# Kernel optimization log

Measured on AMD Instinct MI355X. Metric: run time of the kernel, lower is better.

## Reference

```python
import jax, jax.numpy as jnp
import numpy as np

# levels for the auction iterations: j = 7..-1 gives level = -4^j, j = -2 gives level = 0
_LEVEL_JS = list(range(7, -3, -1))


def approx_match(xyz1, xyz2):
    # xyz1: [B,N,3], xyz2: [B,M,3] -> soft match matrix [B,N,M]
    B, N, _ = xyz1.shape
    M = xyz2.shape[1]
    multiL = 1.0 if N >= M else float(M // N)
    multiR = float(N // M) if N >= M else 1.0
    # pairwise squared distances [B,N,M]
    d2 = jnp.sum((xyz1[:, :, None, :] - xyz2[:, None, :, :]) ** 2, axis=-1)
    levels = jnp.array([0.0 if j == -2 else -(4.0 ** j) for j in _LEVEL_JS],
                       dtype=xyz1.dtype)

    def step(carry, level):
        match, remainL, remainR = carry
        w = jnp.exp(level * d2) * remainR[:, None, :]                      # [B,N,M]
        # row-normalize to each left point's remaining mass
        w = w * (remainL / (jnp.sum(w, axis=2) + 1e-9))[:, :, None]
        # clip columns to right points' remaining capacity
        ss = jnp.sum(w, axis=1) + 1e-9                                     # [B,M]
        w = w * jnp.minimum(remainR / ss, 1.0)[:, None, :]
        match = match + w
        remainL = jnp.maximum(remainL - jnp.sum(w, axis=2), 0.0)
        remainR = jnp.maximum(remainR - jnp.sum(w, axis=1), 0.0)
        return (match, remainL, remainR), None

    init = (jnp.zeros_like(d2),
            jnp.full((B, N), multiL, dtype=d2.dtype),
            jnp.full((B, M), multiR, dtype=d2.dtype))
    (match, _, _), _ = jax.lax.scan(step, init, levels)
    return match


def match_cost(xyz1, xyz2, match):
    # cost[b] = sum_{k,l} match[b,k,l] * ||xyz1[b,k] - xyz2[b,l]||
    d = jnp.sqrt(jnp.sum((xyz1[:, :, None, :] - xyz2[:, None, :, :]) ** 2, axis=-1))
    return jnp.sum(match * d, axis=(1, 2))


def setup_inputs() -> dict:
    key = jax.random.key(0)
    k1, k2 = jax.random.split(key)
    B, N, M = 8, 2048, 2048
    input1 = jax.random.normal(k1, (B, N, 3), dtype=jnp.float32)
    input2 = jax.random.normal(k2, (B, M, 3), dtype=jnp.float32)
    return {"input1": input1, "input2": input2}


def reference(input1, input2):
    match = approx_match(input1, input2)
    return match_cost(input1, input2, match)
```

## Files before the change

### kernel.cpp

```cpp
#include <hip/hip_runtime.h>
#include <hip/hip_fp16.h>


#define BATCH 8
#define NPTS 2048
#define MPTS 2048
#define BLOCK 1024
#define ROWS 64
#define BLOCKS_PER_BATCH 32
#define NSUB 8
#define SUBTGT (BLOCKS_PER_BATCH / NSUB)
#define NSYNC 21
#define PAD 16
#define SKIP_THR (-130.0f)
#define LOG2E 1.44269504088896340736f

__device__ __forceinline__ float fast_exp2(float x) {
  return __builtin_amdgcn_exp2f(x);
}
__device__ __forceinline__ float fast_sqrt(float a) {
  return __builtin_amdgcn_sqrtf(a);
}
__device__ __forceinline__ float packh2(float c, float r) {
  __half2 h = __halves2half2(__float2half_rn(c), __float2half_rn(r));
  return __builtin_bit_cast(float, h);
}

__device__ __forceinline__ float cohLoad(const float* p) {
  return __hip_atomic_load((float*)p, __ATOMIC_RELAXED,
                           __HIP_MEMORY_SCOPE_AGENT);
}
__device__ __forceinline__ void cohStore(float* p, float v) {
  __hip_atomic_store(p, v, __ATOMIC_RELAXED, __HIP_MEMORY_SCOPE_AGENT);
}

__device__ __forceinline__ void batch_barrier(unsigned* base, int bid) {
  __syncthreads();
  if (threadIdx.x == 0) {
    __hip_atomic_fetch_add(base + (bid & (NSUB - 1)) * PAD, 1u,
                           __ATOMIC_RELAXED, __HIP_MEMORY_SCOPE_AGENT);
  }
  if (threadIdx.x < NSUB) {
    int guard = 0;
    while (__hip_atomic_load(base + threadIdx.x * PAD, __ATOMIC_RELAXED,
                             __HIP_MEMORY_SCOPE_AGENT) < (unsigned)SUBTGT) {
      __builtin_amdgcn_s_sleep(2);
      if (++guard > (1 << 22)) break;
    }
  }
  asm volatile("" ::: "memory");
  __syncthreads();
}

__device__ __forceinline__ void wave_interval(float& lo, float& hi) {
#pragma unroll
  for (int s = 1; s < 64; s <<= 1) {
    lo = fminf(lo, __shfl_xor(lo, s, 64));
    hi = fmaxf(hi, __shfl_xor(hi, s, 64));
  }
}

__device__ __forceinline__ void load8L(const float4* sA, int r0,
                                       float* x, float* y, float* z) {
#pragma unroll
  for (int j = 0; j < 8; ++j) {
    float4 v = sA[r0 + j];
    x[j] = v.x; y[j] = v.y; z[j] = v.z;
  }
}

__device__ __forceinline__ void sweep2T_fuse(
    float nc, int tid, int t0, const float* rsG, float* wpB,
    float4* sA, const float4* sP, const float2* sTileN, float* sRR) {
  sA[tid].w = cohLoad(rsG + tid);
  sA[tid + 1024].w = cohLoad(rsG + tid + 1024);
  __syncthreads();
  const int m_idx = tid >> 4, c = tid & 15;
  const float4 pm = sP[t0 + m_idx];
  float mlo = pm.x, mhi = pm.x;
  wave_interval(mlo, mhi);
  float part = 0.f;
  for (int ch = 0; ch < 32; ++ch) {
    float2 tn = sTileN[ch];
    float gap = fmaxf(0.f, fmaxf(tn.x - mhi, mlo - tn.y));
    if (nc * gap * gap < SKIP_THR) continue;
    int nb = ch * 64 + c;
#pragma unroll
    for (int j = 0; j < 4; ++j) {
      float4 v = sA[nb + 16 * j];
      float dx = v.x - pm.x, dy = v.y - pm.y, dz = v.z - pm.z;
      float d2 = __builtin_fmaf(dx, dx, __builtin_fmaf(dy, dy, dz * dz));
      part = __builtin_fmaf(fast_exp2(nc * d2), v.w, part);
    }
  }
  part += __shfl_xor(part, 1, 64);
  part += __shfl_xor(part, 2, 64);
  part += __shfl_xor(part, 4, 64);
  part += __shfl_xor(part, 8, 64);
  if (c == 0) {
    float t1v = part;
    float rr = sRR[m_idx];
    float colsum = rr * t1v;
    float cs = fminf(rr / (colsum + 1e-9f), 1.0f);
    float ccv = rr * cs;
    float rn = fmaxf(rr - colsum * cs, 0.f);
    cohStore(wpB + t0 + m_idx, packh2(ccv, rn));
    sRR[m_idx] = rn;
  }
}

__global__ __launch_bounds__(BLOCK) void emd_fused_kernel(
    const float* __restrict__ xyz1, const float* __restrict__ xyz2,
    float* __restrict__ out, float* __restrict__ rowscaleG,
    float* __restrict__ wPack, float* __restrict__ R9acc,
    float* __restrict__ t9, float* __restrict__ outAcc,
    unsigned* __restrict__ ctr) {
  extern __shared__ __align__(16) float4 sDyn[];
  float4* sA = sDyn;
  float4* sP = sDyn + 2048;
  unsigned* sKeyA = (unsigned*)(sDyn + 2048);
  unsigned* sKeyB = ((unsigned*)(sDyn + 2048)) + 2048;

  __shared__ float sRedS[ROWS * 4];
  __shared__ float sRedC[ROWS * 4];
  __shared__ float sRedR[ROWS * 4];
  __shared__ float sCost[ROWS];
  __shared__ float sRowScale[ROWS];
  __shared__ float sRemainL[ROWS];
  __shared__ float sRR[ROWS];
  __shared__ float2 sTileM[128];
  __shared__ float2 sTileN[32];

  const int tid = threadIdx.x;
  const int bid = blockIdx.x;
  const int b = bid >> 5;
  const int t0 = (bid & 31) * ROWS;
  const bool desig = (bid & 31) == 0;
  const int wave = tid >> 6, lane = tid & 63;
  const int mq = wave & 3;
  const int rh = wave >> 2;
  const size_t bM = (size_t)b * MPTS;
  float costAcc = 0.f;

  float* rsG = rowscaleG + (size_t)b * NPTS;
  float* wpB = wPack + bM;
  const float* p1 = xyz1 + (size_t)b * NPTS * 3;
  const float* p2 = xyz2 + bM * 3;
#define CTRB(s) (ctr + (size_t)(((s) * BATCH + b) * NSUB) * PAD)

  for (int e = tid; e < 2048; e += 1024) {
    unsigned u1 = __builtin_bit_cast(unsigned, p1[e * 3]);
    u1 = (u1 & 0x80000000u) ? ~u1 : (u1 | 0x80000000u);
    sKeyA[e] = (u1 & 0xFFFFF800u) | (unsigned)e;
    unsigned u2 = __builtin_bit_cast(unsigned, p2[e * 3]);
    u2 = (u2 & 0x80000000u) ? ~u2 : (u2 | 0x80000000u);
    sKeyB[e] = (u2 & 0xFFFFF800u) | (unsigned)e;
  }
  for (unsigned k = 2; k <= 2048; k <<= 1) {
    for (unsigned j = k >> 1; j > 0; j >>= 1) {
      __syncthreads();
      for (int e = tid; e < 2048; e += 1024) {
        int l = e ^ (int)j;
        if (l > e) {
          bool up = ((e & (int)k) == 0);
          unsigned a = sKeyA[e], bv = sKeyA[l];
          if ((a > bv) == up) { sKeyA[e] = bv; sKeyA[l] = a; }
          unsigned a2 = sKeyB[e], b2 = sKeyB[l];
          if ((a2 > b2) == up) { sKeyB[e] = b2; sKeyB[l] = a2; }
        }
      }
    }
  }
  __syncthreads();
  {
    int iA0 = sKeyA[tid] & 2047, iA1 = sKeyA[tid + 1024] & 2047;
    int iB0 = sKeyB[tid] & 2047, iB1 = sKeyB[tid + 1024] & 2047;
    __syncthreads();
    sA[tid]        = make_float4(p1[iA0*3], p1[iA0*3+1], p1[iA0*3+2], 0.f);
    sA[tid + 1024] = make_float4(p1[iA1*3], p1[iA1*3+1], p1[iA1*3+2], 0.f);
    sP[tid]        = make_float4(p2[iB0*3], p2[iB0*3+1], p2[iB0*3+2], 0.f);
    sP[tid + 1024] = make_float4(p2[iB1*3], p2[iB1*3+1], p2[iB1*3+2], 0.f);
  }
  if (tid < ROWS) sRR[tid] = 1.0f;
  if (desig && tid == 0) {
    cohStore(R9acc + b * PAD, 0.f);
    cohStore(t9 + b * PAD, 0.f);
    cohStore(outAcc + b * PAD, 0.f);
  }
  __syncthreads();
  if (tid < 128) {
    float lo = sP[tid * 16].x, hi = lo;
    for (int i = 1; i < 16; ++i) {
      float x = sP[tid * 16 + i].x;
      lo = fminf(lo, x); hi = fmaxf(hi, x);
    }
    sTileM[tid] = make_float2(lo, hi);
  } else if (tid < 160) {
    int t = tid - 128;
    float lo = sA[t * 64].x, hi = lo;
    for (int i = 1; i < 64; ++i) {
      float x = sA[t * 64 + i].x;
      lo = fminf(lo, x); hi = fmaxf(hi, x);
    }
    sTileN[t] = make_float2(lo, hi);
  }
  __syncthreads();

  const float nc0 = -16384.0f * LOG2E;
  {
    const int ph = lane >> 1, rg = lane & 1;
    float x1a[8], y1a[8], z1a[8], acc[8];
    load8L(sA, t0 + rh * 16 + rg * 8, x1a, y1a, z1a);
#pragma unroll
    for (int j = 0; j < 8; ++j) acc[j] = 0.f;
    float rlo = x1a[0], rhi = x1a[0];
#pragma unroll
    for (int j = 1; j < 8; ++j) {
      rlo = fminf(rlo, x1a[j]); rhi = fmaxf(rhi, x1a[j]);
    }
    wave_interval(rlo, rhi);
    const int mb = mq * 512 + ph;
    for (int it = 0; it < 16; ++it) {
      int tb = mq * 32 + it * 2;
      float lo = sTileM[tb].x, hi = sTileM[tb + 1].y;
      float gap = fmaxf(0.f, fmaxf(lo - rhi, rlo - hi));
      if (nc0 * gap * gap < SKIP_THR) continue;
      float4 v = sP[mb + it * 32];
#pragma unroll
      for (int j = 0; j < 8; ++j) {
        float dx = x1a[j] - v.x, dy = y1a[j] - v.y, dz = z1a[j] - v.z;
        float d2 = __builtin_fmaf(dx, dx, __builtin_fmaf(dy, dy, dz * dz));
        acc[j] += fast_exp2(nc0 * d2);
      }
    }
#pragma unroll
    for (int j = 0; j < 8; ++j) {
      acc[j] += __shfl_xor(acc[j], 2, 64);
      acc[j] += __shfl_xor(acc[j], 4, 64);
      acc[j] += __shfl_xor(acc[j], 8, 64);
      acc[j] += __shfl_xor(acc[j], 16, 64);
      acc[j] += __shfl_xor(acc[j], 32, 64);
    }
    if (lane < 2) {
#pragma unroll
      for (int j = 0; j < 8; ++j)
        sRedS[(rh * 16 + rg * 8 + j) * 4 + mq] = acc[j];
    }
    __syncthreads();
    if (tid < ROWS) {
      float s = sRedS[tid * 4] + sRedS[tid * 4 + 1] + sRedS[tid * 4 + 2] +
                sRedS[tid * 4 + 3];
      float rs = 1.0f / (s + 1e-9f);
      sRowScale[tid] = rs;
      cohStore(rsG + t0 + tid, rs);
    }
  }
  batch_barrier(CTRB(0), bid);
  sweep2T_fuse(nc0, tid, t0, rsG, wpB, sA, sP, sTileN, sRR);
  batch_barrier(CTRB(1), bid);

  float x1[4], y1[4], z1[4];
  {
    int r0 = t0 + rh * 16 + (lane & 3) * 4;
#pragma unroll
    for (int j = 0; j < 4; ++j) {
      float4 v = sA[r0 + j];
      x1[j] = v.x; y1[j] = v.y; z1[j] = v.z;
    }
  }
  float rlo = fminf(fminf(x1[0], x1[1]), fminf(x1[2], x1[3]));
  float rhi = fmaxf(fmaxf(x1[0], x1[1]), fmaxf(x1[2], x1[3]));
  wave_interval(rlo, rhi);
  const int phc = lane >> 2, rgc = lane & 3;
  const int mbc = mq * 512 + phc;

  float nc2 = -4096.0f * LOG2E;
  for (int l = 0; l < 9; ++l) {
    const bool LAST = (l == 8);
#pragma unroll
    for (int k = 0; k < 2; ++k) {
      int m = tid + k * 1024;
      sP[m].w = cohLoad(wpB + m);
    }
    __syncthreads();
    float accS[4] = {0.f, 0.f, 0.f, 0.f};
    float accC[4] = {0.f, 0.f, 0.f, 0.f};
    float accR[4] = {0.f, 0.f, 0.f, 0.f};
    for (int it = 0; it < 32; ++it) {
      float2 tm = sTileM[mq * 32 + it];
      float gap = fmaxf(0.f, fmaxf(tm.x - rhi, rlo - tm.y));
      if (nc2 * gap * gap < SKIP_THR) continue;
      float4 v = sP[mbc + it * 16];
      __half2 h = __builtin_bit_cast(__half2, v.w);
      float cc = __low2float(h);
      float rr = __high2float(h);
#pragma unroll
      for (int j = 0; j < 4; ++j) {
        float dx = x1[j] - v.x, dy = y1[j] - v.y, dz = z1[j] - v.z;
        float d2 = __builtin_fmaf(dx, dx, __builtin_fmaf(dy, dy, dz * dz));
        float sq = fast_sqrt(d2);
        float e2 = fast_exp2(nc2 * d2);
        float e2s = e2 * e2;
        float e1 = e2s * e2s;
        float t = e1 * cc;
        accS[j] += t;
        accC[j] = __builtin_fmaf(t, sq, accC[j]);
        accR[j] = __builtin_fmaf(e2, rr, accR[j]);
      }
    }
#pragma unroll
    for (int j = 0; j < 4; ++j) {
      accS[j] += __shfl_xor(accS[j], 4, 64);
      accS[j] += __shfl_xor(accS[j], 8, 64);
      accS[j] += __shfl_xor(accS[j], 16, 64);
      accS[j] += __shfl_xor(accS[j], 32, 64);
      accC[j] += __shfl_xor(accC[j], 4, 64);
      accC[j] += __shfl_xor(accC[j], 8, 64);
      accC[j] += __shfl_xor(accC[j], 16, 64);
      accC[j] += __shfl_xor(accC[j], 32, 64);
      accR[j] += __shfl_xor(accR[j], 4, 64);
      accR[j] += __shfl_xor(accR[j], 8, 64);
      accR[j] += __shfl_xor(accR[j], 16, 64);
      accR[j] += __shfl_xor(accR[j], 32, 64);
    }
    if (lane < 4) {
#pragma unroll
      for (int j = 0; j < 4; ++j) {
        int row = rh * 16 + rgc * 4 + j;
        sRedS[row * 4 + mq] = accS[j];
        sRedC[row * 4 + mq] = accC[j];
        sRedR[row * 4 + mq] = accR[j];
      }
    }
    __syncthreads();
    if (tid < ROWS) {
      float S2 = sRedS[tid * 4] + sRedS[tid * 4 + 1] + sRedS[tid * 4 + 2] +
                 sRedS[tid * 4 + 3];
      float C = sRedC[tid * 4] + sRedC[tid * 4 + 1] + sRedC[tid * 4 + 2] +
                sRedC[tid * 4 + 3];
      float R = sRedR[tid * 4] + sRedR[tid * 4 + 1] + sRedR[tid * 4 + 2] +
                sRedR[tid * 4 + 3];
      if (LAST) R = cohLoad(R9acc + b * PAD);
      float rs = sRowScale[tid];
      float rl = (l == 0) ? 1.0f : sRemainL[tid];
      float rlN = fmaxf(rl - rs * S2, 0.f);
      sRemainL[tid] = rlN;
      float rsN = rlN / (R + 1e-9f);
      sRowScale[tid] = rsN;
      if (!LAST) cohStore(rsG + t0 + tid, rsN);
      sCost[tid] = rs * C;
    }
    __syncthreads();
    if (tid == 0) {
      float t = 0.f;
#pragma unroll
      for (int i = 0; i < ROWS; ++i) t += sCost[i];
      costAcc += t;
      if (LAST) {
        float r = 0.f;
#pragma unroll
        for (int i = 0; i < ROWS; ++i) r += sRowScale[i];
        atomicAdd(t9 + b * PAD, r);
      }
    }
    if (!LAST) {
      batch_barrier(CTRB(2 + 2 * l), bid);
      sweep2T_fuse(nc2, tid, t0, rsG, wpB, sA, sP, sTileN, sRR);
      if (l == 7) {
        __syncthreads();
        if (tid == 0) {
          float r9 = 0.f;
#pragma unroll
          for (int i = 0; i < ROWS; ++i) r9 += sRR[i];
          atomicAdd(R9acc + b * PAD, r9);
        }
      }
      batch_barrier(CTRB(3 + 2 * l), bid);
      nc2 *= 0.25f;
    }
  }
  batch_barrier(CTRB(18), bid);

  if (tid < ROWS) {
    float rr = sRR[tid];
    float t1s = cohLoad(t9 + b * PAD);
    float w = rr * fminf(rr / (__builtin_fmaf(rr, t1s, 1e-9f)), 1.0f);
    cohStore(wpB + t0 + tid, w);
  }
  batch_barrier(CTRB(19), bid);

  {
#pragma unroll
    for (int k = 0; k < 2; ++k) {
      int m = tid + k * 1024;
      sP[m].w = cohLoad(wpB + m);
    }
    __syncthreads();
    const int ph = lane >> 1, rg = lane & 1;
    float x1a[8], y1a[8], z1a[8], acc[8];
    load8L(sA, t0 + rh * 16 + rg * 8, x1a, y1a, z1a);
#pragma unroll
    for (int j = 0; j < 8; ++j) acc[j] = 0.f;
    const int mb = mq * 512 + ph;
#pragma unroll 2
    for (int it = 0; it < 16; ++it) {
      float4 v = sP[mb + it * 32];
#pragma unroll
      for (int j = 0; j < 8; ++j) {
        float dx = x1a[j] - v.x, dy = y1a[j] - v.y, dz = z1a[j] - v.z;
        float d2 = __builtin_fmaf(dx, dx, __builtin_fmaf(dy, dy, dz * dz));
        acc[j] = __builtin_fmaf(fast_sqrt(d2), v.w, acc[j]);
      }
    }
#pragma unroll
    for (int j = 0; j < 8; ++j) {
      acc[j] += __shfl_xor(acc[j], 2, 64);
      acc[j] += __shfl_xor(acc[j], 4, 64);
      acc[j] += __shfl_xor(acc[j], 8, 64);
      acc[j] += __shfl_xor(acc[j], 16, 64);
      acc[j] += __shfl_xor(acc[j], 32, 64);
    }
    if (lane < 2) {
#pragma unroll
      for (int j = 0; j < 8; ++j)
        sRedS[(rh * 16 + rg * 8 + j) * 4 + mq] = acc[j];
    }
    __syncthreads();
    if (tid < ROWS) {
      float C = sRedS[tid * 4] + sRedS[tid * 4 + 1] + sRedS[tid * 4 + 2] +
                sRedS[tid * 4 + 3];
      sCost[tid] = sRowScale[tid] * C;
    }
    __syncthreads();
    if (tid == 0) {
      float t = 0.f;
#pragma unroll
      for (int i = 0; i < ROWS; ++i) t += sCost[i];
      costAcc += t;
      atomicAdd(outAcc + b * PAD, costAcc);
    }
  }
  batch_barrier(CTRB(20), bid);
  if (desig && tid == 0) out[b] = cohLoad(outAcc + b * PAD);
#undef CTRB
}

extern "C" void kernel_launch(void* const* d_in, const int* in_sizes, int n_in,
                              void* d_out, int out_size, void* d_ws, size_t ws_size,
                              hipStream_t stream) {
  const float* xyz1 = (const float*)d_in[0];
  const float* xyz2 = (const float*)d_in[1];
  float* out = (float*)d_out;
  float* ws = (float*)d_ws;

  const int BM = BATCH * MPTS;
  float* rowscaleG = ws;
  float* wPack     = ws + BM;
  float* R9acc     = ws + 2 * BM;
  float* t9        = ws + 2 * BM + BATCH * PAD;
  float* outAcc    = ws + 2 * BM + 2 * BATCH * PAD;
  unsigned* ctr    = (unsigned*)(ws + 2 * BM + 3 * BATCH * PAD);

  static bool attrSet = false;
  if (!attrSet) {
    hipFuncSetAttribute((const void*)emd_fused_kernel,
                        hipFuncAttributeMaxDynamicSharedMemorySize, 65536);
    attrSet = true;
  }

  hipMemsetAsync(ctr, 0, (size_t)NSYNC * BATCH * NSUB * PAD * sizeof(unsigned),
                 stream);

  void* args[] = {(void*)&xyz1, (void*)&xyz2, (void*)&out, (void*)&rowscaleG,
                  (void*)&wPack, (void*)&R9acc, (void*)&t9, (void*)&outAcc,
                  (void*)&ctr};
  hipLaunchKernel((const void*)emd_fused_kernel,
                  dim3(BATCH * (NPTS / ROWS)), dim3(BLOCK), args,
                  65536, stream);
}
```

Baseline: 353.2 us.

## Interleave sorted row tiles across blocks and stripe column tiles across waves

Each block now owns four 16-point groups strided by 32 groups through the x-sorted order, instead of one contiguous 64-point slice. Waves likewise take interleaved column tiles rather than a contiguous quarter. Under the distance-based tile skipping, contiguous slices gave very uneven work: blocks near the middle of the sort did most of the exp evaluations. Interleaving is meant to balance that work across blocks and waves so batch barriers wait less on stragglers. The cost is a wider x-range per wave, which may make skipping less effective for wave-level intervals.

New measurement: 319.0 us. -9.7%, faster.

```diff
diff --git a/kernel.cpp b/kernel.cpp
--- a/kernel.cpp
+++ b/kernel.cpp
@@ -70,13 +70,14 @@
 }
 
 __device__ __forceinline__ void sweep2T_fuse(
-    float nc, int tid, int t0, const float* rsG, float* wpB,
+    float nc, int tid, int bslot, const float* rsG, float* wpB,
     float4* sA, const float4* sP, const float2* sTileN, float* sRR) {
   sA[tid].w = cohLoad(rsG + tid);
   sA[tid + 1024].w = cohLoad(rsG + tid + 1024);
   __syncthreads();
   const int m_idx = tid >> 4, c = tid & 15;
-  const float4 pm = sP[t0 + m_idx];
+  const int gm = (bslot + (m_idx >> 4) * 32) * 16 + (m_idx & 15);
+  const float4 pm = sP[gm];
   float mlo = pm.x, mhi = pm.x;
   wave_interval(mlo, mhi);
   float part = 0.f;
@@ -104,7 +105,7 @@
     float cs = fminf(rr / (colsum + 1e-9f), 1.0f);
     float ccv = rr * cs;
     float rn = fmaxf(rr - colsum * cs, 0.f);
-    cohStore(wpB + t0 + m_idx, packh2(ccv, rn));
+    cohStore(wpB + gm, packh2(ccv, rn));
     sRR[m_idx] = rn;
   }
 }
@@ -134,13 +135,14 @@
   const int tid = threadIdx.x;
   const int bid = blockIdx.x;
   const int b = bid >> 5;
-  const int t0 = (bid & 31) * ROWS;
-  const bool desig = (bid & 31) == 0;
+  const int bslot = bid & 31;
+  const bool desig = bslot == 0;
   const int wave = tid >> 6, lane = tid & 63;
   const int mq = wave & 3;
   const int rh = wave >> 2;
   const size_t bM = (size_t)b * MPTS;
   float costAcc = 0.f;
+#define GB(g) ((bslot + (g) * 32) * 16)
 
   float* rsG = rowscaleG + (size_t)b * NPTS;
   float* wpB = wPack + bM;
@@ -210,7 +212,7 @@
   {
     const int ph = lane >> 1, rg = lane & 1;
     float x1a[8], y1a[8], z1a[8], acc[8];
-    load8L(sA, t0 + rh * 16 + rg * 8, x1a, y1a, z1a);
+    load8L(sA, GB(rh) + rg * 8, x1a, y1a, z1a);
 #pragma unroll
     for (int j = 0; j < 8; ++j) acc[j] = 0.f;
     float rlo = x1a[0], rhi = x1a[0];
@@ -219,13 +221,12 @@
       rlo = fminf(rlo, x1a[j]); rhi = fmaxf(rhi, x1a[j]);
     }
     wave_interval(rlo, rhi);
-    const int mb = mq * 512 + ph;
     for (int it = 0; it < 16; ++it) {
-      int tb = mq * 32 + it * 2;
-      float lo = sTileM[tb].x, hi = sTileM[tb + 1].y;
+      int t2 = it * 4 + mq;
+      float lo = sTileM[2 * t2].x, hi = sTileM[2 * t2 + 1].y;
       float gap = fmaxf(0.f, fmaxf(lo - rhi, rlo - hi));
       if (nc0 * gap * gap < SKIP_THR) continue;
-      float4 v = sP[mb + it * 32];
+      float4 v = sP[t2 * 32 + ph];
 #pragma unroll
       for (int j = 0; j < 8; ++j) {
         float dx = x1a[j] - v.x, dy = y1a[j] - v.y, dz = z1a[j] - v.z;
@@ -252,16 +253,16 @@
                 sRedS[tid * 4 + 3];
       float rs = 1.0f / (s + 1e-9f);
       sRowScale[tid] = rs;
-      cohStore(rsG + t0 + tid, rs);
+      cohStore(rsG + GB(tid >> 4) + (tid & 15), rs);
     }
   }
   batch_barrier(CTRB(0), bid);
-  sweep2T_fuse(nc0, tid, t0, rsG, wpB, sA, sP, sTileN, sRR);
+  sweep2T_fuse(nc0, tid, bslot, rsG, wpB, sA, sP, sTileN, sRR);
   batch_barrier(CTRB(1), bid);
 
   float x1[4], y1[4], z1[4];
   {
-    int r0 = t0 + rh * 16 + (lane & 3) * 4;
+    int r0 = GB(rh) + (lane & 3) * 4;
 #pragma unroll
     for (int j = 0; j < 4; ++j) {
       float4 v = sA[r0 + j];
@@ -272,7 +273,6 @@
   float rhi = fmaxf(fmaxf(x1[0], x1[1]), fmaxf(x1[2], x1[3]));
   wave_interval(rlo, rhi);
   const int phc = lane >> 2, rgc = lane & 3;
-  const int mbc = mq * 512 + phc;
 
   float nc2 = -4096.0f * LOG2E;
   for (int l = 0; l < 9; ++l) {
@@ -287,10 +287,11 @@
     float accC[4] = {0.f, 0.f, 0.f, 0.f};
     float accR[4] = {0.f, 0.f, 0.f, 0.f};
     for (int it = 0; it < 32; ++it) {
-      float2 tm = sTileM[mq * 32 + it];
+      int t = it * 4 + mq;
+      float2 tm = sTileM[t];
       float gap = fmaxf(0.f, fmaxf(tm.x - rhi, rlo - tm.y));
       if (nc2 * gap * gap < SKIP_THR) continue;
-      float4 v = sP[mbc + it * 16];
+      float4 v = sP[t * 16 + phc];
       __half2 h = __builtin_bit_cast(__half2, v.w);
       float cc = __low2float(h);
       float rr = __high2float(h);
@@ -302,9 +303,9 @@
         float e2 = fast_exp2(nc2 * d2);
         float e2s = e2 * e2;
         float e1 = e2s * e2s;
-        float t = e1 * cc;
-        accS[j] += t;
-        accC[j] = __builtin_fmaf(t, sq, accC[j]);
+        float t2 = e1 * cc;
+        accS[j] += t2;
+        accC[j] = __builtin_fmaf(t2, sq, accC[j]);
         accR[j] = __builtin_fmaf(e2, rr, accR[j]);
       }
     }
@@ -347,7 +348,7 @@
       sRemainL[tid] = rlN;
       float rsN = rlN / (R + 1e-9f);
       sRowScale[tid] = rsN;
-      if (!LAST) cohStore(rsG + t0 + tid, rsN);
+      if (!LAST) cohStore(rsG + GB(tid >> 4) + (tid & 15), rsN);
       sCost[tid] = rs * C;
     }
     __syncthreads();
@@ -365,7 +366,7 @@
     }
     if (!LAST) {
       batch_barrier(CTRB(2 + 2 * l), bid);
-      sweep2T_fuse(nc2, tid, t0, rsG, wpB, sA, sP, sTileN, sRR);
+      sweep2T_fuse(nc2, tid, bslot, rsG, wpB, sA, sP, sTileN, sRR);
       if (l == 7) {
         __syncthreads();
         if (tid == 0) {
@@ -385,7 +386,7 @@
     float rr = sRR[tid];
     float t1s = cohLoad(t9 + b * PAD);
     float w = rr * fminf(rr / (__builtin_fmaf(rr, t1s, 1e-9f)), 1.0f);
-    cohStore(wpB + t0 + tid, w);
+    cohStore(wpB + GB(tid >> 4) + (tid & 15), w);
   }
   batch_barrier(CTRB(19), bid);
 
@@ -398,7 +399,7 @@
     __syncthreads();
     const int ph = lane >> 1, rg = lane & 1;
     float x1a[8], y1a[8], z1a[8], acc[8];
-    load8L(sA, t0 + rh * 16 + rg * 8, x1a, y1a, z1a);
+    load8L(sA, GB(rh) + rg * 8, x1a, y1a, z1a);
 #pragma unroll
     for (int j = 0; j < 8; ++j) acc[j] = 0.f;
     const int mb = mq * 512 + ph;
@@ -443,6 +444,7 @@
   batch_barrier(CTRB(20), bid);
   if (desig && tid == 0) out[b] = cohLoad(outAcc + b * PAD);
 #undef CTRB
+#undef GB
 }
 
 extern "C" void kernel_launch(void* const* d_in, const int* in_sizes, int n_in,
```
